# Kernel tuning notes

Measured on AMD Instinct MI355X. Metric: run time of the kernel, lower is better.

The kernel has to match this reference:

```python
import jax, jax.numpy as jnp
import numpy as np

N_NODES = 50000
N_EDGES = 500000
IN_DIM = 256
HIDDEN = 128
HEADS = 4
N_CLS = 10
N_GRAPHS = 512
NEG_SLOPE = 0.2  # PyG GATConv default leaky-relu slope


def _glorot(key, shape):
    fan_in, fan_out = shape[0], shape[-1]
    lim = jnp.sqrt(6.0 / (fan_in + fan_out))
    return jax.random.uniform(key, shape, jnp.float32, -lim, lim)


def setup_inputs() -> dict:
    key = jax.random.key(0)
    ks = jax.random.split(key, 12)
    x = jax.random.normal(ks[0], (N_NODES, IN_DIM), jnp.float32)
    edge_index = jax.random.randint(ks[1], (2, N_EDGES), 0, N_NODES, jnp.int64)
    batch = jnp.sort(jax.random.randint(ks[2], (N_NODES,), 0, N_GRAPHS, jnp.int64))
    HC = HIDDEN * HEADS
    return {
        "x": x,
        "edge_index": edge_index,
        "batch": batch,
        "W1": _glorot(ks[3], (IN_DIM, HC)),
        "a_src1": _glorot(ks[4], (HEADS, HIDDEN)) * 0.1,
        "a_dst1": _glorot(ks[5], (HEADS, HIDDEN)) * 0.1,
        "b1": jnp.zeros((HC,), jnp.float32),
        "W2": _glorot(ks[6], (HC, HC)),
        "a_src2": _glorot(ks[7], (HEADS, HIDDEN)) * 0.1,
        "a_dst2": _glorot(ks[8], (HEADS, HIDDEN)) * 0.1,
        "b2": jnp.zeros((HC,), jnp.float32),
        "Wc": _glorot(ks[9], (HC, N_CLS)),
        "bc": jnp.zeros((N_CLS,), jnp.float32),
    }


def _gat_layer(x, src, dst, W, a_src, a_dst, b):
    """PyG GATConv (concat=True, self-loops already appended, eval mode)."""
    N = x.shape[0]
    h = (x @ W).reshape(N, HEADS, -1)                 # [N, H, C]
    alpha_s = jnp.einsum('nhc,hc->nh', h, a_src)       # [N, H]
    alpha_d = jnp.einsum('nhc,hc->nh', h, a_dst)       # [N, H]
    e = jax.nn.leaky_relu(alpha_s[src] + alpha_d[dst], NEG_SLOPE)  # [E, H]
    # segment softmax over incoming edges of each dst node
    m = jax.ops.segment_max(e, dst, num_segments=N)
    ex = jnp.exp(e - m[dst])
    denom = jax.ops.segment_sum(ex, dst, num_segments=N)
    alpha = ex / (denom[dst] + 1e-16)                  # [E, H]
    out = jax.ops.segment_sum(alpha[:, :, None] * h[src], dst, num_segments=N)
    return out.reshape(N, -1) + b                      # [N, H*C]


def reference(x, edge_index, batch, W1, a_src1, a_dst1, b1,
              W2, a_src2, a_dst2, b2, Wc, bc):
    N = x.shape[0]
    loop = jnp.arange(N, dtype=edge_index.dtype)
    src = jnp.concatenate([edge_index[0], loop])
    dst = jnp.concatenate([edge_index[1], loop])
    h = jax.nn.relu(_gat_layer(x, src, dst, W1, a_src1, a_dst1, b1))
    h = jax.nn.relu(_gat_layer(h, src, dst, W2, a_src2, a_dst2, b2))
    # global mean pool over graphs
    sums = jax.ops.segment_sum(h, batch, num_segments=N_GRAPHS)
    cnt = jax.ops.segment_sum(jnp.ones((N,), h.dtype), batch, num_segments=N_GRAPHS)
    hg = sums / jnp.maximum(cnt, 1.0)[:, None]         # [G, H*C]
    return hg @ Wc + bc                                # [G, n_cls]
```

## Files before the change

kernel.cpp:

```cpp
#include <hip/hip_runtime.h>

#define NN      50000
#define NE      500000
#define NET     550000
#define IND     256
#define HC      512
#define NH      4
#define NG      512
#define NCLS    10

typedef __attribute__((ext_vector_type(8))) _Float16 f16x8;
typedef __attribute__((ext_vector_type(4))) float f32x4;
typedef __attribute__((ext_vector_type(2))) float f32x2;
typedef __attribute__((ext_vector_type(4))) ushort us4;

__device__ __forceinline__ ushort f2bf(float x) {
    unsigned u = __float_as_uint(x);
    u += 0x7fffu + ((u >> 16) & 1u);
    return (ushort)(u >> 16);
}
__device__ __forceinline__ float bf2f(ushort h) {
    return __uint_as_float((unsigned)h << 16);
}
__device__ __forceinline__ ushort f2h(float x) {
    union { _Float16 h; ushort u; } cv;
    cv.h = (_Float16)x;
    return cv.u;
}

__device__ __forceinline__ void gload_lds16(const void* g, void* s) {
    __builtin_amdgcn_global_load_lds(
        (const __attribute__((address_space(1))) unsigned*)g,
        (__attribute__((address_space(3))) unsigned*)s, 16, 0, 0);
}

__global__ __launch_bounds__(256) void k_gemm_f16(
    const ushort* __restrict__ A, const ushort* __restrict__ BT,
    const float* __restrict__ a_srcv, const float* __restrict__ a_dstv,
    unsigned char* __restrict__ Cf8, float* __restrict__ as_b,
    float* __restrict__ ad_b, int M, int K)
{
    __shared__ __align__(16) ushort As[64 * 64];
    __shared__ __align__(16) ushort Bs[128 * 64];
    __shared__ float sred[2][64];

    const int tid = threadIdx.x;
    const int nwg = gridDim.x;
    const int orig = blockIdx.x;
    const int q = nwg >> 3, r = nwg & 7, xcd = orig & 7;
    const int wgid = (xcd < r ? xcd * (q + 1) : r * (q + 1) + (xcd - r) * q) + (orig >> 3);
    const int bm = (wgid >> 2) * 64;
    const int bn = (wgid & 3) * 128;

    const int l = tid & 63;
    const int w = tid >> 6;
    const int wm = (w >> 1) * 32, wn = (w & 1) * 64;
    const int fr = l & 15;
    const int fk = (l >> 4) * 8;

    if (tid < 64) { sred[0][tid] = 0.f; sred[1][tid] = 0.f; }

    f32x4 zero = {0.f, 0.f, 0.f, 0.f};
    f32x4 acc[2][4];
#pragma unroll
    for (int m = 0; m < 2; ++m)
#pragma unroll
        for (int n = 0; n < 4; ++n) acc[m][n] = zero;

    const int nsteps = K >> 6;
    const int wbase = (tid & 0xC0) << 4;

    for (int ks = 0; ks < nsteps; ++ks) {
        int k0 = ks << 6;
#pragma unroll
        for (int i = 0; i < 2; ++i) {
            int c = i * 256 + tid;
            int row = c >> 3;
            int col16 = (c & 7) ^ (row & 7);
            int arow = bm + row; arow = arow < M ? arow : M - 1;
            gload_lds16(A + (size_t)arow * K + k0 + (col16 << 3),
                        (char*)As + i * 4096 + wbase);
        }
#pragma unroll
        for (int i = 0; i < 4; ++i) {
            int c = i * 256 + tid;
            int j = c >> 3;
            int col16 = (c & 7) ^ (j & 7);
            gload_lds16(BT + (size_t)(bn + j) * K + k0 + (col16 << 3),
                        (char*)Bs + i * 4096 + wbase);
        }
        __syncthreads();
#pragma unroll
        for (int kk = 0; kk < 64; kk += 32) {
            f16x8 a[2], b[4];
            int kb = (kk + fk) >> 3;
#pragma unroll
            for (int m = 0; m < 2; ++m) {
                int row = wm + m * 16 + fr;
                a[m] = *(const f16x8*)((const char*)As + row * 128 + ((kb ^ (row & 7)) << 4));
            }
#pragma unroll
            for (int n = 0; n < 4; ++n) {
                int col = wn + n * 16 + fr;
                b[n] = *(const f16x8*)((const char*)Bs + col * 128 + ((kb ^ (col & 7)) << 4));
            }
#pragma unroll
            for (int m = 0; m < 2; ++m)
#pragma unroll
                for (int n = 0; n < 4; ++n)
                    acc[m][n] = __builtin_amdgcn_mfma_f32_16x16x32_f16(a[m], b[n], acc[m][n], 0, 0, 0);
        }
        __syncthreads();
    }

    const int hh = bn >> 7;
    float asl[4], adl[4];
#pragma unroll
    for (int n = 0; n < 4; ++n) {
        int c = wn + n * 16 + fr;
        asl[n] = a_srcv[hh * 128 + c];
        adl[n] = a_dstv[hh * 128 + c];
    }
    const int rbase = (l >> 4) * 4;
#pragma unroll
    for (int m = 0; m < 2; ++m) {
#pragma unroll
        for (int rr = 0; rr < 4; ++rr) {
            int rloc = wm + m * 16 + rbase + rr;
            int rowi = bm + rloc;
            float ps = 0.f, pd = 0.f;
#pragma unroll
            for (int n = 0; n < 4; ++n) {
                float v = acc[m][n][rr];
                ps += v * asl[n];
                pd += v * adl[n];
                if (rowi < M) {
                    int pk = __builtin_amdgcn_cvt_pk_fp8_f32(v, v, 0, false);
                    Cf8[(size_t)rowi * HC + bn + wn + n * 16 + fr] = (unsigned char)pk;
                }
            }
#pragma unroll
            for (int off = 1; off < 16; off <<= 1) {
                ps += __shfl_xor(ps, off, 64);
                pd += __shfl_xor(pd, off, 64);
            }
            if (fr == 0) {
                atomicAdd(&sred[0][rloc], ps);
                atomicAdd(&sred[1][rloc], pd);
            }
        }
    }
    __syncthreads();
    if (tid < 64) {
        int rowi = bm + tid;
        if (rowi < M) {
            as_b[rowi * 4 + hh] = sred[0][tid];
            ad_b[rowi * 4 + hh] = sred[1][tid];
        }
    }
}

__global__ void k_cvt_f16(const float* __restrict__ in, ushort* __restrict__ o,
                          int n4) {
    int i = blockIdx.x * blockDim.x + threadIdx.x;
    if (i >= n4) return;
    float4 v = ((const float4*)in)[i];
    ushort4 h;
    h.x = f2h(v.x); h.y = f2h(v.y); h.z = f2h(v.z); h.w = f2h(v.w);
    ((ushort4*)o)[i] = h;
}

__global__ void k_cvt_wT(const float* __restrict__ W, ushort* __restrict__ hT,
                         int K, int logK) {
    int id = blockIdx.x * blockDim.x + threadIdx.x;
    if (id >= (HC << logK)) return;
    int nn = id >> logK, k = id & (K - 1);
    hT[id] = f2h(W[(size_t)k * HC + nn]);
}

__global__ void k_deg(const int* __restrict__ ei, int* __restrict__ deg) {
    int e = blockIdx.x * blockDim.x + threadIdx.x;
    if (e >= NET) return;
    int d = (e < NE) ? ei[NE + e] : (e - NE);
    atomicAdd(&deg[d], 1);
}

__global__ __launch_bounds__(256) void k_scan_part(const int* __restrict__ cnt,
                                                   int* __restrict__ bsum, int n) {
    __shared__ int red[256];
    const int tid = threadIdx.x;
    int i = blockIdx.x * 256 + tid;
    red[tid] = (i < n) ? cnt[i] : 0;
    __syncthreads();
#pragma unroll
    for (int d = 128; d; d >>= 1) {
        if (tid < d) red[tid] += red[tid + d];
        __syncthreads();
    }
    if (tid == 0) bsum[blockIdx.x] = red[0];
}

__global__ __launch_bounds__(1024) void k_scan_top(const int* __restrict__ bsum,
                                                   int* __restrict__ boff,
                                                   int* __restrict__ off, int nb, int n) {
    __shared__ int s[1024];
    const int tid = threadIdx.x;
    int v = (tid < nb) ? bsum[tid] : 0;
    s[tid] = v;
    __syncthreads();
    for (int d = 1; d < 1024; d <<= 1) {
        int t = (tid >= d) ? s[tid - d] : 0;
        __syncthreads();
        s[tid] += t;
        __syncthreads();
    }
    if (tid < nb) boff[tid] = s[tid] - v;
    if (tid == nb - 1) off[n] = s[tid];
}

__global__ __launch_bounds__(256) void k_scan_out(const int* __restrict__ cnt,
                                                  const int* __restrict__ boff,
                                                  int* __restrict__ off, int n) {
    __shared__ int s[256];
    const int tid = threadIdx.x;
    int i = blockIdx.x * 256 + tid;
    int v = (i < n) ? cnt[i] : 0;
    s[tid] = v;
    __syncthreads();
    for (int d = 1; d < 256; d <<= 1) {
        int t = (tid >= d) ? s[tid - d] : 0;
        __syncthreads();
        s[tid] += t;
        __syncthreads();
    }
    if (i < n) off[i] = boff[blockIdx.x] + s[tid] - v;
}

__global__ void k_fill(const int* __restrict__ ei,
                       const int* __restrict__ rowptr,
                       int* __restrict__ fillcnt,
                       int* __restrict__ colsrc) {
    int e = blockIdx.x * blockDim.x + threadIdx.x;
    if (e >= NET) return;
    int s, d;
    if (e < NE) { s = ei[e]; d = ei[NE + e]; } else { s = d = e - NE; }
    int pos = rowptr[d] + atomicAdd(&fillcnt[d], 1);
    colsrc[pos] = s;
}

__global__ __launch_bounds__(256) void k_stats(
    const float* __restrict__ as, const float* __restrict__ ad,
    const int* __restrict__ rowptr, const int* __restrict__ colsrc,
    float* __restrict__ alpha, float* __restrict__ dinv, int N)
{
    const int n = blockIdx.x * 64 + (threadIdx.x >> 2);
    if (n >= N) return;
    const int h = threadIdx.x & 3;
    const int beg = rowptr[n], end = rowptr[n + 1];
    const float adn = ad[n * 4 + h];
    float sum = 0.f;
    for (int e = beg; e < end; ++e) {
        float ev = as[colsrc[e] * 4 + h] + adn;
        ev = ev > 0.f ? ev : 0.2f * ev;
        float a = __expf(ev);
        alpha[(size_t)e * 4 + h] = a;
        sum += a;
    }
    dinv[n * 4 + h] = 1.0f / (sum + 1e-16f);
}

__global__ __launch_bounds__(256) void k_gather(
    const unsigned char* __restrict__ zf8, const float* __restrict__ alpha,
    const float* __restrict__ dinv, const int* __restrict__ rowptr,
    const int* __restrict__ colsrc, const float* __restrict__ bias,
    ushort* __restrict__ o16, int obf16)
{
    const int npb = NN >> 2;
    const int hp = blockIdx.x / npb;
    const int sub = threadIdx.x >> 5;
    const int node = (blockIdx.x % npb) * 4 + (sub >> 1);
    const int head = hp * 2 + (sub & 1);
    const int lane = threadIdx.x & 31;
    const int beg = rowptr[node], end = rowptr[node + 1];
    const unsigned char* __restrict__ zh = zf8 + head * 128 + (lane << 2);

    float ax = 0.f, ay = 0.f, az = 0.f, aw = 0.f;
    int e = beg;
    for (; e + 4 <= end; e += 4) {
        int s0 = colsrc[e], s1 = colsrc[e + 1], s2 = colsrc[e + 2], s3 = colsrc[e + 3];
        float a0 = alpha[(size_t)e * 4 + head];
        float a1 = alpha[(size_t)(e + 1) * 4 + head];
        float a2 = alpha[(size_t)(e + 2) * 4 + head];
        float a3 = alpha[(size_t)(e + 3) * 4 + head];
        unsigned u0 = *(const unsigned*)&zh[(size_t)s0 * HC];
        unsigned u1 = *(const unsigned*)&zh[(size_t)s1 * HC];
        unsigned u2 = *(const unsigned*)&zh[(size_t)s2 * HC];
        unsigned u3 = *(const unsigned*)&zh[(size_t)s3 * HC];
        f32x2 l0 = __builtin_amdgcn_cvt_pk_f32_fp8(u0, false);
        f32x2 h0 = __builtin_amdgcn_cvt_pk_f32_fp8(u0, true);
        f32x2 l1 = __builtin_amdgcn_cvt_pk_f32_fp8(u1, false);
        f32x2 h1 = __builtin_amdgcn_cvt_pk_f32_fp8(u1, true);
        f32x2 l2 = __builtin_amdgcn_cvt_pk_f32_fp8(u2, false);
        f32x2 h2 = __builtin_amdgcn_cvt_pk_f32_fp8(u2, true);
        f32x2 l3 = __builtin_amdgcn_cvt_pk_f32_fp8(u3, false);
        f32x2 h3 = __builtin_amdgcn_cvt_pk_f32_fp8(u3, true);
        ax += a0 * l0.x + a1 * l1.x + a2 * l2.x + a3 * l3.x;
        ay += a0 * l0.y + a1 * l1.y + a2 * l2.y + a3 * l3.y;
        az += a0 * h0.x + a1 * h1.x + a2 * h2.x + a3 * h3.x;
        aw += a0 * h0.y + a1 * h1.y + a2 * h2.y + a3 * h3.y;
    }
    for (; e < end; ++e) {
        int s0 = colsrc[e];
        float a0 = alpha[(size_t)e * 4 + head];
        unsigned u0 = *(const unsigned*)&zh[(size_t)s0 * HC];
        f32x2 l0 = __builtin_amdgcn_cvt_pk_f32_fp8(u0, false);
        f32x2 h0 = __builtin_amdgcn_cvt_pk_f32_fp8(u0, true);
        ax += a0 * l0.x; ay += a0 * l0.y; az += a0 * h0.x; aw += a0 * h0.y;
    }
    const float di = dinv[node * 4 + head];
    const int col = head * 128 + (lane << 2);
    float4 bv = *(const float4*)&bias[col];
    float rx = fmaxf(ax * di + bv.x, 0.f), ry = fmaxf(ay * di + bv.y, 0.f);
    float rz = fmaxf(az * di + bv.z, 0.f), rw = fmaxf(aw * di + bv.w, 0.f);
    us4 h;
    if (obf16) {
        h.x = f2bf(rx); h.y = f2bf(ry); h.z = f2bf(rz); h.w = f2bf(rw);
    } else {
        h.x = f2h(rx); h.y = f2h(ry); h.z = f2h(rz); h.w = f2h(rw);
    }
    __builtin_nontemporal_store(h, (us4*)&o16[(size_t)node * HC + col]);
}

__global__ void k_gcnt(const int* __restrict__ batch, int* __restrict__ gcnt) {
    int n = blockIdx.x * blockDim.x + threadIdx.x;
    if (n < NN) atomicAdd(&gcnt[batch[n]], 1);
}

__global__ __launch_bounds__(128) void k_pool(const ushort* __restrict__ h,
                                              const int* __restrict__ goff,
                                              const int* __restrict__ gcnt,
                                              float* __restrict__ hg) {
    const int g = blockIdx.x;
    const int tid = threadIdx.x;
    const int beg = goff[g];
    const int cnt = gcnt[g];
    float4 acc = make_float4(0.f, 0.f, 0.f, 0.f);
    for (int r = beg; r < beg + cnt; ++r) {
        ushort4 v = *(const ushort4*)&h[(size_t)r * HC + (tid << 2)];
        acc.x += bf2f(v.x); acc.y += bf2f(v.y);
        acc.z += bf2f(v.z); acc.w += bf2f(v.w);
    }
    float inv = 1.0f / (float)max(cnt, 1);
    *(float4*)&hg[(size_t)g * HC + (tid << 2)] =
        make_float4(acc.x * inv, acc.y * inv, acc.z * inv, acc.w * inv);
}

__global__ __launch_bounds__(64) void k_cls(const float* __restrict__ hg,
                                            const float* __restrict__ Wc,
                                            const float* __restrict__ bc,
                                            float* __restrict__ out) {
    const int g = blockIdx.x;
    const int lane = threadIdx.x;
#pragma unroll 1
    for (int cls = 0; cls < NCLS; ++cls) {
        float p = 0.f;
#pragma unroll
        for (int j = 0; j < 8; ++j) {
            int c = lane + j * 64;
            p += hg[(size_t)g * HC + c] * Wc[c * NCLS + cls];
        }
#pragma unroll
        for (int off = 32; off; off >>= 1) p += __shfl_down(p, off, 64);
        if (lane == 0) out[g * NCLS + cls] = p + bc[cls];
    }
}

extern "C" void kernel_launch(void* const* d_in, const int* in_sizes, int n_in,
                              void* d_out, int out_size, void* d_ws, size_t ws_size,
                              hipStream_t stream) {
    const float* x     = (const float*)d_in[0];
    const int*   ei    = (const int*)d_in[1];
    const int*   batch = (const int*)d_in[2];
    const float* W1    = (const float*)d_in[3];
    const float* asrc1 = (const float*)d_in[4];
    const float* adst1 = (const float*)d_in[5];
    const float* b1    = (const float*)d_in[6];
    const float* W2    = (const float*)d_in[7];
    const float* asrc2 = (const float*)d_in[8];
    const float* adst2 = (const float*)d_in[9];
    const float* b2    = (const float*)d_in[10];
    const float* Wc    = (const float*)d_in[11];
    const float* bc    = (const float*)d_in[12];
    float* out = (float*)d_out;
    (void)in_sizes; (void)n_in; (void)out_size; (void)ws_size;

    char* R = (char*)d_ws;
    const size_t MB512 = (size_t)NN * HC;
    unsigned char* zf8 = (unsigned char*)R;
    ushort* xf16  = (ushort*)(R + MB512);
    ushort* h1f16 = (ushort*)(R + MB512);
    ushort* h2b   = (ushort*)(R + MB512);

    char* w = R + MB512 * 3;
    size_t off = 0;
    auto alloc = [&](size_t bytes) {
        void* p = w + off;
        off += (bytes + 255) & ~(size_t)255;
        return p;
    };
    float* as_b = (float*)alloc((size_t)NN * NH * 4);
    float* ad_b = (float*)alloc((size_t)NN * NH * 4);
    float* dinv = (float*)alloc((size_t)NN * NH * 4);
    int* rowptr = (int*)alloc((size_t)(NN + 1) * 4);
    int* deg    = (int*)alloc((size_t)NN * 4);
    int* colsrc = (int*)alloc((size_t)NET * 4);
    int* gcnt   = (int*)alloc((size_t)NG * 4);
    int* goff   = (int*)alloc((size_t)(NG + 1) * 4);
    int* bsum   = (int*)alloc((size_t)1024 * 4);
    int* boff   = (int*)alloc((size_t)1024 * 4);
    float* hg   = (float*)alloc((size_t)NG * HC * 4);
    ushort* W1T = (ushort*)alloc((size_t)HC * IND * 2);
    ushort* W2T = (ushort*)alloc((size_t)HC * HC * 2);
    float* alpha = (float*)alloc((size_t)NET * NH * 4);

    const int EB = 256, EG = (NET + EB - 1) / EB;
    const int MT = (NN + 63) / 64;
    const int GG = 2 * (NN >> 2);
    const int NB_N = (NN + 255) / 256;
    const int NB_G = (NG + 255) / 256;

    k_cvt_f16<<<(NN * IND / 4 + 255) / 256, 256, 0, stream>>>(x, xf16, NN * IND / 4);
    k_cvt_wT<<<(HC * IND + 255) / 256, 256, 0, stream>>>(W1, W1T, IND, 8);
    k_cvt_wT<<<(HC * HC + 255) / 256, 256, 0, stream>>>(W2, W2T, HC, 9);

    hipMemsetAsync(deg, 0, (size_t)NN * 4, stream);
    k_deg<<<EG, EB, 0, stream>>>(ei, deg);
    k_scan_part<<<NB_N, 256, 0, stream>>>(deg, bsum, NN);
    k_scan_top<<<1, 1024, 0, stream>>>(bsum, boff, rowptr, NB_N, NN);
    k_scan_out<<<NB_N, 256, 0, stream>>>(deg, boff, rowptr, NN);
    hipMemsetAsync(deg, 0, (size_t)NN * 4, stream);
    k_fill<<<EG, EB, 0, stream>>>(ei, rowptr, deg, colsrc);

    hipMemsetAsync(gcnt, 0, (size_t)NG * 4, stream);
    k_gcnt<<<(NN + 255) / 256, 256, 0, stream>>>(batch, gcnt);
    k_scan_part<<<NB_G, 256, 0, stream>>>(gcnt, bsum, NG);
    k_scan_top<<<1, 1024, 0, stream>>>(bsum, boff, goff, NB_G, NG);
    k_scan_out<<<NB_G, 256, 0, stream>>>(gcnt, boff, goff, NG);

    k_gemm_f16<<<MT * 4, 256, 0, stream>>>(xf16, W1T, asrc1, adst1,
                                           zf8, as_b, ad_b, NN, IND);
    k_stats<<<(NN + 63) / 64, 256, 0, stream>>>(as_b, ad_b, rowptr, colsrc,
                                                alpha, dinv, NN);
    k_gather<<<GG, 256, 0, stream>>>(zf8, alpha, dinv, rowptr, colsrc, b1,
                                     h1f16, 0);

    k_gemm_f16<<<MT * 4, 256, 0, stream>>>(h1f16, W2T, asrc2, adst2,
                                           zf8, as_b, ad_b, NN, HC);
    k_stats<<<(NN + 63) / 64, 256, 0, stream>>>(as_b, ad_b, rowptr, colsrc,
                                                alpha, dinv, NN);
    k_gather<<<GG, 256, 0, stream>>>(zf8, alpha, dinv, rowptr, colsrc, b2,
                                     h2b, 1);

    k_pool<<<NG, 128, 0, stream>>>(h2b, goff, gcnt, hg);
    k_cls<<<NG, 64, 0, stream>>>(hg, Wc, bc, out);
}
```

Before: 408.2 us.

## Store CSR column indices as ushort and attention weights as fp16, unroll gather by 8

Shrinks the CSR source-index array from int to ushort and the per-edge attention coefficients from fp32 to fp16, which halves that traffic in the stats and gather kernels. The gather loop is unrolled to 8 edges, with all loads issued before the FMAs to raise memory-level parallelism. However, node indices go up to 49999, which fits in 16 bits, so the ushort truncation is safe only because NN is below 65536. The fp16 alpha adds rounding error, and exp of large scores could overflow fp16 since no max subtraction is done.

```diff
diff --git a/kernel.cpp b/kernel.cpp
--- a/kernel.cpp
+++ b/kernel.cpp
@@ -26,6 +26,11 @@
     union { _Float16 h; ushort u; } cv;
     cv.h = (_Float16)x;
     return cv.u;
+}
+__device__ __forceinline__ float h2f(ushort u) {
+    union { ushort u; _Float16 h; } cv;
+    cv.u = u;
+    return (float)cv.h;
 }
 
 __device__ __forceinline__ void gload_lds16(const void* g, void* s) {
@@ -239,19 +244,19 @@
 __global__ void k_fill(const int* __restrict__ ei,
                        const int* __restrict__ rowptr,
                        int* __restrict__ fillcnt,
-                       int* __restrict__ colsrc) {
+                       ushort* __restrict__ colsrc) {
     int e = blockIdx.x * blockDim.x + threadIdx.x;
     if (e >= NET) return;
     int s, d;
     if (e < NE) { s = ei[e]; d = ei[NE + e]; } else { s = d = e - NE; }
     int pos = rowptr[d] + atomicAdd(&fillcnt[d], 1);
-    colsrc[pos] = s;
+    colsrc[pos] = (ushort)s;
 }
 
 __global__ __launch_bounds__(256) void k_stats(
     const float* __restrict__ as, const float* __restrict__ ad,
-    const int* __restrict__ rowptr, const int* __restrict__ colsrc,
-    float* __restrict__ alpha, float* __restrict__ dinv, int N)
+    const int* __restrict__ rowptr, const ushort* __restrict__ colsrc,
+    ushort* __restrict__ alpha, float* __restrict__ dinv, int N)
 {
     const int n = blockIdx.x * 64 + (threadIdx.x >> 2);
     if (n >= N) return;
@@ -260,19 +265,19 @@
     const float adn = ad[n * 4 + h];
     float sum = 0.f;
     for (int e = beg; e < end; ++e) {
-        float ev = as[colsrc[e] * 4 + h] + adn;
+        float ev = as[(int)colsrc[e] * 4 + h] + adn;
         ev = ev > 0.f ? ev : 0.2f * ev;
         float a = __expf(ev);
-        alpha[(size_t)e * 4 + h] = a;
+        alpha[(size_t)e * 4 + h] = f2h(a);
         sum += a;
     }
     dinv[n * 4 + h] = 1.0f / (sum + 1e-16f);
 }
 
 __global__ __launch_bounds__(256) void k_gather(
-    const unsigned char* __restrict__ zf8, const float* __restrict__ alpha,
+    const unsigned char* __restrict__ zf8, const ushort* __restrict__ alpha,
     const float* __restrict__ dinv, const int* __restrict__ rowptr,
-    const int* __restrict__ colsrc, const float* __restrict__ bias,
+    const ushort* __restrict__ colsrc, const float* __restrict__ bias,
     ushort* __restrict__ o16, int obf16)
 {
     const int npb = NN >> 2;
@@ -286,32 +291,41 @@
 
     float ax = 0.f, ay = 0.f, az = 0.f, aw = 0.f;
     int e = beg;
-    for (; e + 4 <= end; e += 4) {
-        int s0 = colsrc[e], s1 = colsrc[e + 1], s2 = colsrc[e + 2], s3 = colsrc[e + 3];
-        float a0 = alpha[(size_t)e * 4 + head];
-        float a1 = alpha[(size_t)(e + 1) * 4 + head];
-        float a2 = alpha[(size_t)(e + 2) * 4 + head];
-        float a3 = alpha[(size_t)(e + 3) * 4 + head];
+    for (; e + 8 <= end; e += 8) {
+        int s[8];
+        float a[8];
+        unsigned u[8];
+#pragma unroll
+        for (int j = 0; j < 8; ++j) {
+            s[j] = colsrc[e + j];
+            a[j] = h2f(alpha[(size_t)(e + j) * 4 + head]);
+        }
+#pragma unroll
+        for (int j = 0; j < 8; ++j) u[j] = *(const unsigned*)&zh[(size_t)s[j] * HC];
+#pragma unroll
+        for (int j = 0; j < 8; ++j) {
+            f32x2 lo = __builtin_amdgcn_cvt_pk_f32_fp8(u[j], false);
+            f32x2 hi = __builtin_amdgcn_cvt_pk_f32_fp8(u[j], true);
+            ax += a[j] * lo.x; ay += a[j] * lo.y;
+            az += a[j] * hi.x; aw += a[j] * hi.y;
+        }
+    }
+    for (; e + 2 <= end; e += 2) {
+        int s0 = colsrc[e], s1 = colsrc[e + 1];
+        float a0 = h2f(alpha[(size_t)e * 4 + head]);
+        float a1 = h2f(alpha[(size_t)(e + 1) * 4 + head]);
         unsigned u0 = *(const unsigned*)&zh[(size_t)s0 * HC];
         unsigned u1 = *(const unsigned*)&zh[(size_t)s1 * HC];
-        unsigned u2 = *(const unsigned*)&zh[(size_t)s2 * HC];
-        unsigned u3 = *(const unsigned*)&zh[(size_t)s3 * HC];
         f32x2 l0 = __builtin_amdgcn_cvt_pk_f32_fp8(u0, false);
         f32x2 h0 = __builtin_amdgcn_cvt_pk_f32_fp8(u0, true);
         f32x2 l1 = __builtin_amdgcn_cvt_pk_f32_fp8(u1, false);
         f32x2 h1 = __builtin_amdgcn_cvt_pk_f32_fp8(u1, true);
-        f32x2 l2 = __builtin_amdgcn_cvt_pk_f32_fp8(u2, false);
-        f32x2 h2 = __builtin_amdgcn_cvt_pk_f32_fp8(u2, true);
-        f32x2 l3 = __builtin_amdgcn_cvt_pk_f32_fp8(u3, false);
-        f32x2 h3 = __builtin_amdgcn_cvt_pk_f32_fp8(u3, true);
-        ax += a0 * l0.x + a1 * l1.x + a2 * l2.x + a3 * l3.x;
-        ay += a0 * l0.y + a1 * l1.y + a2 * l2.y + a3 * l3.y;
-        az += a0 * h0.x + a1 * h1.x + a2 * h2.x + a3 * h3.x;
-        aw += a0 * h0.y + a1 * h1.y + a2 * h2.y + a3 * h3.y;
-    }
-    for (; e < end; ++e) {
+        ax += a0 * l0.x + a1 * l1.x; ay += a0 * l0.y + a1 * l1.y;
+        az += a0 * h0.x + a1 * h1.x; aw += a0 * h0.y + a1 * h1.y;
+    }
+    if (e < end) {
         int s0 = colsrc[e];
-        float a0 = alpha[(size_t)e * 4 + head];
+        float a0 = h2f(alpha[(size_t)e * 4 + head]);
         unsigned u0 = *(const unsigned*)&zh[(size_t)s0 * HC];
         f32x2 l0 = __builtin_amdgcn_cvt_pk_f32_fp8(u0, false);
         f32x2 h0 = __builtin_amdgcn_cvt_pk_f32_fp8(u0, true);
@@ -413,7 +427,7 @@
     float* dinv = (float*)alloc((size_t)NN * NH * 4);
     int* rowptr = (int*)alloc((size_t)(NN + 1) * 4);
     int* deg    = (int*)alloc((size_t)NN * 4);
-    int* colsrc = (int*)alloc((size_t)NET * 4);
+    ushort* colsrc = (ushort*)alloc((size_t)NET * 2);
     int* gcnt   = (int*)alloc((size_t)NG * 4);
     int* goff   = (int*)alloc((size_t)(NG + 1) * 4);
     int* bsum   = (int*)alloc((size_t)1024 * 4);
@@ -421,7 +435,7 @@
     float* hg   = (float*)alloc((size_t)NG * HC * 4);
     ushort* W1T = (ushort*)alloc((size_t)HC * IND * 2);
     ushort* W2T = (ushort*)alloc((size_t)HC * HC * 2);
-    float* alpha = (float*)alloc((size_t)NET * NH * 4);
+    ushort* alpha = (ushort*)alloc((size_t)NET * NH * 2);
 
     const int EB = 256, EG = (NET + EB - 1) / EB;
     const int MT = (NN + 63) / 64;
```

After: 394.2 us. 1.04x faster.
